# Kernel tuning notes

Measured on AMD Instinct MI355X. Metric: run time of the kernel, lower is better.

Reference implementation:

```python
import jax, jax.numpy as jnp
import numpy as np

OBS_X, OBS_Y, RADIUS = 40.0, 15.0, 6.0
B = 524288  # batch of states


def setup_inputs() -> dict:
    key = jax.random.key(0)
    ks = jax.random.split(key, 14)
    def lin_w(k, o, i):
        return jax.random.normal(k, (o, i), jnp.float32) * (1.0 / np.sqrt(i))
    return {
        "x": jax.random.normal(ks[0], (B, 5), jnp.float32),
        "sgn": 1,
        "mean": jax.random.normal(ks[1], (5,), jnp.float32),
        "std": jax.random.uniform(ks[2], (5,), jnp.float32, minval=0.5, maxval=1.5),
        "fc1_w": lin_w(ks[3], 128, 5),
        "fc1_b": jax.random.normal(ks[4], (128,), jnp.float32) * 0.1,
        "fc21_w": lin_w(ks[5], 32, 128),
        "fc21_b": jax.random.normal(ks[6], (32,), jnp.float32) * 0.1,
        "fc22_w": lin_w(ks[7], 32, 128),
        "fc22_b": jax.random.normal(ks[8], (32,), jnp.float32) * 0.1,
        "fc31_w": lin_w(ks[9], 2, 32),
        "fc31_b": jax.random.normal(ks[10], (2,), jnp.float32) * 0.1,
        "fc32_w": lin_w(ks[11], 2, 32),
        "fc32_b": jax.random.normal(ks[12], (2,), jnp.float32) * 0.1,
    }


def reference(x, sgn, mean, std, fc1_w, fc1_b, fc21_w, fc21_b,
              fc22_w, fc22_b, fc31_w, fc31_b, fc32_w, fc32_b):
    # --- tiny MLP (DynamicUnicycle2D config: 5 -> 128 -> {32,32} -> {2,2}) ---
    x0 = x * std + mean                                   # de-normalized state [B,5]
    h1 = jax.nn.relu(x @ fc1_w.T + fc1_b)                 # [B,128]
    x21 = jax.nn.relu(h1 @ fc21_w.T + fc21_b)             # [B,32]
    x22 = jax.nn.relu(h1 @ fc22_w.T + fc22_b)             # [B,32]
    x31 = x21 @ fc31_w.T + fc31_b                         # QP linear cost p, [B,2]
    x32 = 4.0 * jax.nn.sigmoid(x22 @ fc32_w.T + fc32_b)   # CBF class-K gains, [B,2]

    # --- CBF derivation (relative degree 2, circular obstacle) ---
    px, py, theta, v = x0[:, 0], x0[:, 1], x0[:, 2], x0[:, 3]
    s, c = jnp.sin(theta), jnp.cos(theta)
    dx, dy = px - OBS_X, py - OBS_Y
    barrier = dx * dx + dy * dy - RADIUS * RADIUS
    barrier_dot = 2.0 * dx * v * c + 2.0 * dy * v * s
    Lf2b = 2.0 * v * v
    LgLfbu1 = -2.0 * dx * v * s + 2.0 * dy * v * c
    LgLfbu2 = 2.0 * dx * c + 2.0 * dy * s
    G = jnp.stack([-LgLfbu1, -LgLfbu2], axis=1)           # [B,2], single row constraint
    h = Lf2b + (x32[:, 0] + x32[:, 1]) * barrier_dot + x32[:, 0] * x32[:, 1] * barrier  # [B]

    # --- batched QP: min 0.5 u^T u + p^T u  s.t.  G u <= h  (Q = I, one constraint)
    # Exact KKT solution: project unconstrained optimum onto the half-space.
    u0 = -x31                                             # unconstrained optimum
    viol = jnp.sum(G * u0, axis=1) - h                    # [B]
    gg = jnp.sum(G * G, axis=1)                           # [B]
    lam = jnp.maximum(viol, 0.0) / (gg + 1e-12)           # active-set multiplier
    u = u0 - lam[:, None] * G                             # [B,2] safe control
    return u
```

## Files before the change

### kernel.cpp

```cpp
#include <hip/hip_runtime.h>
#include <hip/hip_bf16.h>
#include <math.h>

typedef __attribute__((ext_vector_type(8))) _Float16 half8;
typedef __attribute__((ext_vector_type(2))) _Float16 half2v;
typedef __attribute__((ext_vector_type(4))) float f32x4;

#define OBS_X 40.0f
#define OBS_Y 15.0f
#define RADIUS 6.0f
#define TPW 16
#define GRID 512

__device__ __forceinline__ half2v pkrtz(float a, float b) {
    return __builtin_bit_cast(half2v, __builtin_amdgcn_cvt_pkrtz(a, b));
}

__device__ __forceinline__ void split8(const float* v, half8& hi, half8& lo) {
#pragma unroll
    for (int j = 0; j < 8; ++j) {
        _Float16 h = (_Float16)v[j];
        hi[j] = h;
        lo[j] = (_Float16)(v[j] - (float)h);
    }
}

__device__ __forceinline__ void pin(half8& v) {
    f32x4 t = __builtin_bit_cast(f32x4, v);
    asm volatile("" : "+v"(t));
    v = __builtin_bit_cast(half8, t);
}

__global__ __launch_bounds__(256, 2) void barriernet_fused(
    const float* __restrict__ x,
    const float* __restrict__ mean_, const float* __restrict__ std_,
    const float* __restrict__ w1,  const float* __restrict__ b1,
    const float* __restrict__ w21, const float* __restrict__ b21,
    const float* __restrict__ w22, const float* __restrict__ b22,
    const float* __restrict__ w31, const float* __restrict__ b31,
    const float* __restrict__ w32, const float* __restrict__ b32,
    float* __restrict__ out)
{
    __shared__ unsigned char smem[36880];
    const int tid  = threadIdx.x;
    const int lane = tid & 63;
    const int wv   = tid >> 6;
    const int r16  = lane & 15;
    const int g    = lane >> 4;
    unsigned char* h1hi = smem + wv * 8192;
    unsigned char* h1lo = h1hi + 4096;
    const unsigned swz = ((unsigned)(r16 & 7)) << 4;
    const int slot = blockIdx.x * 4 + wv;

    if (tid < 128) {
        float v[8];
#pragma unroll
        for (int j = 0; j < 5; ++j) v[j] = w1[tid * 5 + j];
        v[5] = b1[tid];
        v[6] = 0.f; v[7] = 0.f;
        half8 hi, lo;
        split8(v, hi, lo);
        *(half8*)(smem + 32768 + tid * 16) = hi;
        *(half8*)(smem + 34816 + tid * 16) = lo;
    }
    if (tid == 128) {
        half8 z = {0,0,0,0,0,0,0,0};
        *(half8*)(smem + 36864) = z;
    }

    half8 w2h[4][4], w2l[4][4];
#pragma unroll
    for (int t = 0; t < 4; ++t) {
        const int r = 16 * t + r16;
        const float* src = (r < 32) ? (w21 + r * 128) : (w22 + (r - 32) * 128);
#pragma unroll
        for (int kc = 0; kc < 4; ++kc) {
            const float4 f0 = *(const float4*)(src + kc * 32 + g * 8);
            const float4 f1 = *(const float4*)(src + kc * 32 + g * 8 + 4);
            float v[8];
            v[0] = f0.x; v[1] = f0.y; v[2] = f0.z; v[3] = f0.w;
            v[4] = f1.x; v[5] = f1.y; v[6] = f1.z; v[7] = f1.w;
            split8(v, w2h[t][kc], w2l[t][kc]);
            pin(w2h[t][kc]);
            pin(w2l[t][kc]);
        }
    }

    __syncthreads();

    const float m0 = mean_[0], m1 = mean_[1], m2 = mean_[2], m3 = mean_[3];
    const float sd0 = std_[0], sd1 = std_[1], sd2 = std_[2], sd3 = std_[3];
    const float bb31_0 = b31[0], bb31_1 = b31[1], bb32_0 = b32[0], bb32_1 = b32[1];

    const unsigned awbase = (g < 2) ? 32768u : ((g == 2) ? 34816u : 36864u);
    const unsigned awstep = (g == 3) ? 0u : 16u;

    float xa0, xa1, xa2, xa3, xa4;
    {
        const float* xr = x + (size_t)(slot * TPW * 16 + r16) * 5;
        xa0 = xr[0]; xa1 = xr[1]; xa2 = xr[2]; xa3 = xr[3]; xa4 = xr[4];
    }

#pragma unroll 1
    for (int it = 0; it < TPW; ++it) {
        const int rowbase = (slot * TPW + it) * 16;

        half8 bx = {0,0,0,0,0,0,0,0};
        {
            float xs[5] = {xa0, xa1, xa2, xa3, xa4};
            const bool useL = (g == 1), useZ = (g == 3);
#pragma unroll
            for (int j = 0; j < 5; ++j) {
                _Float16 h = (_Float16)xs[j];
                _Float16 l = (_Float16)(xs[j] - (float)h);
                bx[j] = useZ ? (_Float16)0.f : (useL ? l : h);
            }
            bx[5] = (useZ || useL) ? (_Float16)0.f : (_Float16)1.0f;
        }
        const float xc0 = xa0, xc1 = xa1, xc2 = xa2, xc3 = xa3;

        if (it + 1 < TPW) {
            const float* xr = x + (size_t)(rowbase + 16 + r16) * 5;
            xa0 = xr[0]; xa1 = xr[1]; xa2 = xr[2]; xa3 = xr[3]; xa4 = xr[4];
        }

#pragma unroll
        for (int t8 = 0; t8 < 8; ++t8) {
            const int fr = t8 * 16 + r16;
            const half8 aw = *(const half8*)(smem + awbase + (unsigned)fr * awstep);
            f32x4 acc = {0.f, 0.f, 0.f, 0.f};
            acc = __builtin_amdgcn_mfma_f32_16x16x32_f16(aw, bx, acc, 0, 0, 0);
            float v0 = fmaxf(acc[0], 0.f), v1 = fmaxf(acc[1], 0.f);
            float v2 = fmaxf(acc[2], 0.f), v3 = fmaxf(acc[3], 0.f);
            half2v hA = pkrtz(v0, v1);
            half2v hB = pkrtz(v2, v3);
            half2v lA = pkrtz(v0 - (float)hA[0], v1 - (float)hA[1]);
            half2v lB = pkrtz(v2 - (float)hB[0], v3 - (float)hB[1]);
            const unsigned off = ((unsigned)(32 * t8 + 8 * g)) ^ swz;
            uint2 ph; ph.x = __builtin_bit_cast(unsigned, hA); ph.y = __builtin_bit_cast(unsigned, hB);
            uint2 pl; pl.x = __builtin_bit_cast(unsigned, lA); pl.y = __builtin_bit_cast(unsigned, lB);
            *(uint2*)(h1hi + r16 * 256 + off) = ph;
            *(uint2*)(h1lo + r16 * 256 + off) = pl;
        }

        asm volatile("" ::: "memory");

        half8 ah[4], al[4];
#pragma unroll
        for (int kc = 0; kc < 4; ++kc) {
            const unsigned off = ((unsigned)(kc * 64 + g * 16)) ^ swz;
            ah[kc] = *(const half8*)(h1hi + r16 * 256 + off);
            al[kc] = *(const half8*)(h1lo + r16 * 256 + off);
        }
        f32x4 acc2[4];
#pragma unroll
        for (int t = 0; t < 4; ++t) {
            const float4 bb2 = (t < 2) ? *(const float4*)(b21 + 16 * t + 4 * g)
                                       : *(const float4*)(b22 + 16 * (t - 2) + 4 * g);
            f32x4 a = {bb2.x, bb2.y, bb2.z, bb2.w};
#pragma unroll
            for (int kc = 0; kc < 4; ++kc) {
                a = __builtin_amdgcn_mfma_f32_16x16x32_f16(w2h[t][kc], al[kc], a, 0, 0, 0);
                a = __builtin_amdgcn_mfma_f32_16x16x32_f16(w2l[t][kc], ah[kc], a, 0, 0, 0);
                a = __builtin_amdgcn_mfma_f32_16x16x32_f16(w2h[t][kc], ah[kc], a, 0, 0, 0);
            }
            acc2[t] = a;
        }

        asm volatile("" ::: "memory");

        const f32x4 wA0 = *(const f32x4*)(w31 + 4 * g);
        const f32x4 wA1 = *(const f32x4*)(w31 + 16 + 4 * g);
        const f32x4 wB0 = *(const f32x4*)(w31 + 32 + 4 * g);
        const f32x4 wB1 = *(const f32x4*)(w31 + 48 + 4 * g);
        const f32x4 wC0 = *(const f32x4*)(w32 + 4 * g);
        const f32x4 wC1 = *(const f32x4*)(w32 + 16 + 4 * g);
        const f32x4 wD0 = *(const f32x4*)(w32 + 32 + 4 * g);
        const f32x4 wD1 = *(const f32x4*)(w32 + 48 + 4 * g);
        float p0 = 0.f, p1 = 0.f, p2 = 0.f, p3 = 0.f;
#pragma unroll
        for (int r = 0; r < 4; ++r) {
            float v0 = fmaxf(acc2[0][r], 0.f), v1 = fmaxf(acc2[1][r], 0.f);
            float v2 = fmaxf(acc2[2][r], 0.f), v3 = fmaxf(acc2[3][r], 0.f);
            p0 += wA0[r] * v0 + wA1[r] * v1;
            p1 += wB0[r] * v0 + wB1[r] * v1;
            p2 += wC0[r] * v2 + wC1[r] * v3;
            p3 += wD0[r] * v2 + wD1[r] * v3;
        }
        p0 += __shfl_xor(p0, 16); p0 += __shfl_xor(p0, 32);
        p1 += __shfl_xor(p1, 16); p1 += __shfl_xor(p1, 32);
        p2 += __shfl_xor(p2, 16); p2 += __shfl_xor(p2, 32);
        p3 += __shfl_xor(p3, 16); p3 += __shfl_xor(p3, 32);

        if (lane < 16) {
            const float a31_0 = p0 + bb31_0, a31_1 = p1 + bb31_1;
            const float a32_0 = p2 + bb32_0, a32_1 = p3 + bb32_1;
            const float s0 = 4.0f / (1.0f + __expf(-a32_0));
            const float s1 = 4.0f / (1.0f + __expf(-a32_1));
            const float px = fmaf(xc0, sd0, m0);
            const float py = fmaf(xc1, sd1, m1);
            const float th = fmaf(xc2, sd2, m2);
            const float v  = fmaf(xc3, sd3, m3);
            float sn, cs; __sincosf(th, &sn, &cs);
            const float dx = px - OBS_X, dy = py - OBS_Y;
            const float barrier     = dx * dx + dy * dy - RADIUS * RADIUS;
            const float barrier_dot = 2.f * dx * v * cs + 2.f * dy * v * sn;
            const float Lf2b = 2.f * v * v;
            const float G0 = 2.f * dx * v * sn - 2.f * dy * v * cs;
            const float G1 = -(2.f * dx * cs + 2.f * dy * sn);
            const float h  = Lf2b + (s0 + s1) * barrier_dot + s0 * s1 * barrier;
            const float u00 = -a31_0, u01 = -a31_1;
            const float viol = G0 * u00 + G1 * u01 - h;
            const float gg   = G0 * G0 + G1 * G1;
            const float lam  = fmaxf(viol, 0.f) / (gg + 1e-12f);
            float2 uo = make_float2(fmaf(-lam, G0, u00), fmaf(-lam, G1, u01));
            ((float2*)out)[rowbase + r16] = uo;
        }
    }
}

extern "C" void kernel_launch(void* const* d_in, const int* in_sizes, int n_in,
                              void* d_out, int out_size, void* d_ws, size_t ws_size,
                              hipStream_t stream) {
    const float* x     = (const float*)d_in[0];
    const float* mean_ = (const float*)d_in[2];
    const float* std_  = (const float*)d_in[3];
    const float* w1    = (const float*)d_in[4];
    const float* b1    = (const float*)d_in[5];
    const float* w21   = (const float*)d_in[6];
    const float* b21   = (const float*)d_in[7];
    const float* w22   = (const float*)d_in[8];
    const float* b22   = (const float*)d_in[9];
    const float* w31   = (const float*)d_in[10];
    const float* b31   = (const float*)d_in[11];
    const float* w32   = (const float*)d_in[12];
    const float* b32   = (const float*)d_in[13];

    barriernet_fused<<<GRID, 256, 0, stream>>>(
        x, mean_, std_, w1, b1, w21, b21, w22, b22, w31, b31, w32, b32,
        (float*)d_out);
}
```

Baseline: 133.6 us.

## Move fc2 low-half weights to LDS, raise occupancy, batch epilogue across four tiles

```diff
diff --git a/kernel.cpp b/kernel.cpp
--- a/kernel.cpp
+++ b/kernel.cpp
@@ -9,8 +9,8 @@
 #define OBS_X 40.0f
 #define OBS_Y 15.0f
 #define RADIUS 6.0f
-#define TPW 16
-#define GRID 512
+#define TPW 8
+#define GRID 1024
 
 __device__ __forceinline__ half2v pkrtz(float a, float b) {
     return __builtin_bit_cast(half2v, __builtin_amdgcn_cvt_pkrtz(a, b));
@@ -31,7 +31,7 @@
     v = __builtin_bit_cast(half8, t);
 }
 
-__global__ __launch_bounds__(256, 2) void barriernet_fused(
+__global__ __launch_bounds__(256, 3) void barriernet_fused(
     const float* __restrict__ x,
     const float* __restrict__ mean_, const float* __restrict__ std_,
     const float* __restrict__ w1,  const float* __restrict__ b1,
@@ -41,7 +41,7 @@
     const float* __restrict__ w32, const float* __restrict__ b32,
     float* __restrict__ out)
 {
-    __shared__ unsigned char smem[36880];
+    __shared__ unsigned char smem[53264];
     const int tid  = threadIdx.x;
     const int lane = tid & 63;
     const int wv   = tid >> 6;
@@ -60,15 +60,30 @@
         v[6] = 0.f; v[7] = 0.f;
         half8 hi, lo;
         split8(v, hi, lo);
-        *(half8*)(smem + 32768 + tid * 16) = hi;
-        *(half8*)(smem + 34816 + tid * 16) = lo;
+        *(half8*)(smem + 49152 + tid * 16) = hi;
+        *(half8*)(smem + 51200 + tid * 16) = lo;
     }
     if (tid == 128) {
         half8 z = {0,0,0,0,0,0,0,0};
-        *(half8*)(smem + 36864) = z;
-    }
-
-    half8 w2h[4][4], w2l[4][4];
+        *(half8*)(smem + 53248) = z;
+    }
+
+#pragma unroll
+    for (int m = 0; m < 4; ++m) {
+        const int s = tid * 4 + m;
+        const int f = s >> 6, l = s & 63;
+        const int r = 16 * (f >> 2) + (l & 15);
+        const int k0 = (f & 3) * 32 + (l >> 4) * 8;
+        const float* src = (r < 32) ? (w21 + r * 128 + k0) : (w22 + (r - 32) * 128 + k0);
+        const float4 f0 = *(const float4*)(src);
+        const float4 f1 = *(const float4*)(src + 4);
+        float v[8] = {f0.x, f0.y, f0.z, f0.w, f1.x, f1.y, f1.z, f1.w};
+        half8 hi, lo;
+        split8(v, hi, lo);
+        *(half8*)(smem + 32768 + s * 16) = lo;
+    }
+
+    half8 w2h[4][4];
 #pragma unroll
     for (int t = 0; t < 4; ++t) {
         const int r = 16 * t + r16;
@@ -77,12 +92,10 @@
         for (int kc = 0; kc < 4; ++kc) {
             const float4 f0 = *(const float4*)(src + kc * 32 + g * 8);
             const float4 f1 = *(const float4*)(src + kc * 32 + g * 8 + 4);
-            float v[8];
-            v[0] = f0.x; v[1] = f0.y; v[2] = f0.z; v[3] = f0.w;
-            v[4] = f1.x; v[5] = f1.y; v[6] = f1.z; v[7] = f1.w;
-            split8(v, w2h[t][kc], w2l[t][kc]);
+            float v[8] = {f0.x, f0.y, f0.z, f0.w, f1.x, f1.y, f1.z, f1.w};
+#pragma unroll
+            for (int j = 0; j < 8; ++j) w2h[t][kc][j] = (_Float16)v[j];
             pin(w2h[t][kc]);
-            pin(w2l[t][kc]);
         }
     }
 
@@ -92,14 +105,17 @@
     const float sd0 = std_[0], sd1 = std_[1], sd2 = std_[2], sd3 = std_[3];
     const float bb31_0 = b31[0], bb31_1 = b31[1], bb32_0 = b32[0], bb32_1 = b32[1];
 
-    const unsigned awbase = (g < 2) ? 32768u : ((g == 2) ? 34816u : 36864u);
+    const unsigned awbase = (g < 2) ? 49152u : ((g == 2) ? 51200u : 53248u);
     const unsigned awstep = (g == 3) ? 0u : 16u;
+    const unsigned w2lbase = 32768u + (unsigned)lane * 16u;
 
     float xa0, xa1, xa2, xa3, xa4;
     {
         const float* xr = x + (size_t)(slot * TPW * 16 + r16) * 5;
         xa0 = xr[0]; xa1 = xr[1]; xa2 = xr[2]; xa3 = xr[3]; xa4 = xr[4];
     }
+
+    float P0 = 0.f, P1 = 0.f, P2 = 0.f, P3 = 0.f;
 
 #pragma unroll 1
     for (int it = 0; it < TPW; ++it) {
@@ -117,7 +133,6 @@
             }
             bx[5] = (useZ || useL) ? (_Float16)0.f : (_Float16)1.0f;
         }
-        const float xc0 = xa0, xc1 = xa1, xc2 = xa2, xc3 = xa3;
 
         if (it + 1 < TPW) {
             const float* xr = x + (size_t)(rowbase + 16 + r16) * 5;
@@ -160,8 +175,9 @@
             f32x4 a = {bb2.x, bb2.y, bb2.z, bb2.w};
 #pragma unroll
             for (int kc = 0; kc < 4; ++kc) {
+                const half8 wl = *(const half8*)(smem + w2lbase + (unsigned)((t * 4 + kc) << 10));
                 a = __builtin_amdgcn_mfma_f32_16x16x32_f16(w2h[t][kc], al[kc], a, 0, 0, 0);
-                a = __builtin_amdgcn_mfma_f32_16x16x32_f16(w2l[t][kc], ah[kc], a, 0, 0, 0);
+                a = __builtin_amdgcn_mfma_f32_16x16x32_f16(wl,         ah[kc], a, 0, 0, 0);
                 a = __builtin_amdgcn_mfma_f32_16x16x32_f16(w2h[t][kc], ah[kc], a, 0, 0, 0);
             }
             acc2[t] = a;
@@ -192,15 +208,26 @@
         p2 += __shfl_xor(p2, 16); p2 += __shfl_xor(p2, 32);
         p3 += __shfl_xor(p3, 16); p3 += __shfl_xor(p3, 32);
 
-        if (lane < 16) {
-            const float a31_0 = p0 + bb31_0, a31_1 = p1 + bb31_1;
-            const float a32_0 = p2 + bb32_0, a32_1 = p3 + bb32_1;
+        {
+            const bool sel = (g == (it & 3));
+            P0 = sel ? p0 : P0;
+            P1 = sel ? p1 : P1;
+            P2 = sel ? p2 : P2;
+            P3 = sel ? p3 : P3;
+        }
+
+        if ((it & 3) == 3) {
+            const int row = (slot * TPW + (it - 3)) * 16 + lane;
+            const float* xr = x + (size_t)row * 5;
+            const float e0 = xr[0], e1 = xr[1], e2 = xr[2], e3 = xr[3];
+            const float a31_0 = P0 + bb31_0, a31_1 = P1 + bb31_1;
+            const float a32_0 = P2 + bb32_0, a32_1 = P3 + bb32_1;
             const float s0 = 4.0f / (1.0f + __expf(-a32_0));
             const float s1 = 4.0f / (1.0f + __expf(-a32_1));
-            const float px = fmaf(xc0, sd0, m0);
-            const float py = fmaf(xc1, sd1, m1);
-            const float th = fmaf(xc2, sd2, m2);
-            const float v  = fmaf(xc3, sd3, m3);
+            const float px = fmaf(e0, sd0, m0);
+            const float py = fmaf(e1, sd1, m1);
+            const float th = fmaf(e2, sd2, m2);
+            const float v  = fmaf(e3, sd3, m3);
             float sn, cs; __sincosf(th, &sn, &cs);
             const float dx = px - OBS_X, dy = py - OBS_Y;
             const float barrier     = dx * dx + dy * dy - RADIUS * RADIUS;
@@ -214,7 +241,7 @@
             const float gg   = G0 * G0 + G1 * G1;
             const float lam  = fmaxf(viol, 0.f) / (gg + 1e-12f);
             float2 uo = make_float2(fmaf(-lam, G0, u00), fmaf(-lam, G1, u01));
-            ((float2*)out)[rowbase + r16] = uo;
+            ((float2*)out)[row] = uo;
         }
     }
 }
```

After: 146.0 us. +9.2%, slower.

## Double-buffer fc1 activations in LDS to overlap next tile's fc1 with fc2

Applied to the files above, without the earlier changes.

```diff
diff --git a/kernel.cpp b/kernel.cpp
--- a/kernel.cpp
+++ b/kernel.cpp
@@ -41,14 +41,13 @@
     const float* __restrict__ w32, const float* __restrict__ b32,
     float* __restrict__ out)
 {
-    __shared__ unsigned char smem[36880];
+    __shared__ unsigned char smem[69648];
     const int tid  = threadIdx.x;
     const int lane = tid & 63;
     const int wv   = tid >> 6;
     const int r16  = lane & 15;
     const int g    = lane >> 4;
-    unsigned char* h1hi = smem + wv * 8192;
-    unsigned char* h1lo = h1hi + 4096;
+    unsigned char* h1base = smem + wv * 16384;
     const unsigned swz = ((unsigned)(r16 & 7)) << 4;
     const int slot = blockIdx.x * 4 + wv;
 
@@ -60,12 +59,12 @@
         v[6] = 0.f; v[7] = 0.f;
         half8 hi, lo;
         split8(v, hi, lo);
-        *(half8*)(smem + 32768 + tid * 16) = hi;
-        *(half8*)(smem + 34816 + tid * 16) = lo;
+        *(half8*)(smem + 65536 + tid * 16) = hi;
+        *(half8*)(smem + 67584 + tid * 16) = lo;
     }
     if (tid == 128) {
         half8 z = {0,0,0,0,0,0,0,0};
-        *(half8*)(smem + 36864) = z;
+        *(half8*)(smem + 69632) = z;
     }
 
     half8 w2h[4][4], w2l[4][4];
@@ -92,56 +91,71 @@
     const float sd0 = std_[0], sd1 = std_[1], sd2 = std_[2], sd3 = std_[3];
     const float bb31_0 = b31[0], bb31_1 = b31[1], bb32_0 = b32[0], bb32_1 = b32[1];
 
-    const unsigned awbase = (g < 2) ? 32768u : ((g == 2) ? 34816u : 36864u);
+    const unsigned awbase = (g < 2) ? 65536u : ((g == 2) ? 67584u : 69632u);
     const unsigned awstep = (g == 3) ? 0u : 16u;
+
+#define FC1_TO(BUF, BX)                                                               \
+    {                                                                                 \
+        unsigned char* hhi = h1base + ((unsigned)(BUF) << 13);                        \
+        unsigned char* hlo = hhi + 4096;                                              \
+        _Pragma("unroll")                                                             \
+        for (int t8 = 0; t8 < 8; ++t8) {                                              \
+            const int fr = t8 * 16 + r16;                                             \
+            const half8 aw = *(const half8*)(smem + awbase + (unsigned)fr * awstep);  \
+            f32x4 acc = {0.f, 0.f, 0.f, 0.f};                                         \
+            acc = __builtin_amdgcn_mfma_f32_16x16x32_f16(aw, BX, acc, 0, 0, 0);       \
+            float v0 = fmaxf(acc[0], 0.f), v1 = fmaxf(acc[1], 0.f);                   \
+            float v2 = fmaxf(acc[2], 0.f), v3 = fmaxf(acc[3], 0.f);                   \
+            half2v hA = pkrtz(v0, v1);                                                \
+            half2v hB = pkrtz(v2, v3);                                                \
+            half2v lA = pkrtz(v0 - (float)hA[0], v1 - (float)hA[1]);                  \
+            half2v lB = pkrtz(v2 - (float)hB[0], v3 - (float)hB[1]);                  \
+            const unsigned off = ((unsigned)(32 * t8 + 8 * g)) ^ swz;                 \
+            uint2 ph; ph.x = __builtin_bit_cast(unsigned, hA);                        \
+            ph.y = __builtin_bit_cast(unsigned, hB);                                  \
+            uint2 pl; pl.x = __builtin_bit_cast(unsigned, lA);                        \
+            pl.y = __builtin_bit_cast(unsigned, lB);                                  \
+            *(uint2*)(hhi + r16 * 256 + off) = ph;                                    \
+            *(uint2*)(hlo + r16 * 256 + off) = pl;                                    \
+        }                                                                             \
+    }
+
+#define BUILD_BX(DST, X0, X1, X2, X3, X4)                                             \
+    {                                                                                 \
+        float xs[5] = {X0, X1, X2, X3, X4};                                           \
+        const bool useL = (g == 1), useZ = (g == 3);                                  \
+        _Pragma("unroll")                                                             \
+        for (int j = 0; j < 5; ++j) {                                                 \
+            _Float16 h = (_Float16)xs[j];                                             \
+            _Float16 l = (_Float16)(xs[j] - (float)h);                                \
+            DST[j] = useZ ? (_Float16)0.f : (useL ? l : h);                           \
+        }                                                                             \
+        DST[5] = (useZ || useL) ? (_Float16)0.f : (_Float16)1.0f;                     \
+        DST[6] = (_Float16)0.f; DST[7] = (_Float16)0.f;                               \
+    }
 
     float xa0, xa1, xa2, xa3, xa4;
     {
         const float* xr = x + (size_t)(slot * TPW * 16 + r16) * 5;
         xa0 = xr[0]; xa1 = xr[1]; xa2 = xr[2]; xa3 = xr[3]; xa4 = xr[4];
     }
+    float xc0 = xa0, xc1 = xa1, xc2 = xa2, xc3 = xa3;
+    {
+        half8 bx0;
+        BUILD_BX(bx0, xa0, xa1, xa2, xa3, xa4);
+        FC1_TO(0, bx0);
+    }
+    {
+        const float* xr = x + (size_t)(slot * TPW * 16 + 16 + r16) * 5;
+        xa0 = xr[0]; xa1 = xr[1]; xa2 = xr[2]; xa3 = xr[3]; xa4 = xr[4];
+    }
 
 #pragma unroll 1
     for (int it = 0; it < TPW; ++it) {
+        const int cur = it & 1;
         const int rowbase = (slot * TPW + it) * 16;
-
-        half8 bx = {0,0,0,0,0,0,0,0};
-        {
-            float xs[5] = {xa0, xa1, xa2, xa3, xa4};
-            const bool useL = (g == 1), useZ = (g == 3);
-#pragma unroll
-            for (int j = 0; j < 5; ++j) {
-                _Float16 h = (_Float16)xs[j];
-                _Float16 l = (_Float16)(xs[j] - (float)h);
-                bx[j] = useZ ? (_Float16)0.f : (useL ? l : h);
-            }
-            bx[5] = (useZ || useL) ? (_Float16)0.f : (_Float16)1.0f;
-        }
-        const float xc0 = xa0, xc1 = xa1, xc2 = xa2, xc3 = xa3;
-
-        if (it + 1 < TPW) {
-            const float* xr = x + (size_t)(rowbase + 16 + r16) * 5;
-            xa0 = xr[0]; xa1 = xr[1]; xa2 = xr[2]; xa3 = xr[3]; xa4 = xr[4];
-        }
-
-#pragma unroll
-        for (int t8 = 0; t8 < 8; ++t8) {
-            const int fr = t8 * 16 + r16;
-            const half8 aw = *(const half8*)(smem + awbase + (unsigned)fr * awstep);
-            f32x4 acc = {0.f, 0.f, 0.f, 0.f};
-            acc = __builtin_amdgcn_mfma_f32_16x16x32_f16(aw, bx, acc, 0, 0, 0);
-            float v0 = fmaxf(acc[0], 0.f), v1 = fmaxf(acc[1], 0.f);
-            float v2 = fmaxf(acc[2], 0.f), v3 = fmaxf(acc[3], 0.f);
-            half2v hA = pkrtz(v0, v1);
-            half2v hB = pkrtz(v2, v3);
-            half2v lA = pkrtz(v0 - (float)hA[0], v1 - (float)hA[1]);
-            half2v lB = pkrtz(v2 - (float)hB[0], v3 - (float)hB[1]);
-            const unsigned off = ((unsigned)(32 * t8 + 8 * g)) ^ swz;
-            uint2 ph; ph.x = __builtin_bit_cast(unsigned, hA); ph.y = __builtin_bit_cast(unsigned, hB);
-            uint2 pl; pl.x = __builtin_bit_cast(unsigned, lA); pl.y = __builtin_bit_cast(unsigned, lB);
-            *(uint2*)(h1hi + r16 * 256 + off) = ph;
-            *(uint2*)(h1lo + r16 * 256 + off) = pl;
-        }
+        unsigned char* bhi = h1base + ((unsigned)cur << 13);
+        unsigned char* blo = bhi + 4096;
 
         asm volatile("" ::: "memory");
 
@@ -149,9 +163,22 @@
 #pragma unroll
         for (int kc = 0; kc < 4; ++kc) {
             const unsigned off = ((unsigned)(kc * 64 + g * 16)) ^ swz;
-            ah[kc] = *(const half8*)(h1hi + r16 * 256 + off);
-            al[kc] = *(const half8*)(h1lo + r16 * 256 + off);
-        }
+            ah[kc] = *(const half8*)(bhi + r16 * 256 + off);
+            al[kc] = *(const half8*)(blo + r16 * 256 + off);
+        }
+
+        float xn0 = xc0, xn1 = xc1, xn2 = xc2, xn3 = xc3;
+        if (it + 1 < TPW) {
+            xn0 = xa0; xn1 = xa1; xn2 = xa2; xn3 = xa3;
+            half8 bxn;
+            BUILD_BX(bxn, xa0, xa1, xa2, xa3, xa4);
+            if (it + 2 < TPW) {
+                const float* xr = x + (size_t)(rowbase + 32 + r16) * 5;
+                xa0 = xr[0]; xa1 = xr[1]; xa2 = xr[2]; xa3 = xr[3]; xa4 = xr[4];
+            }
+            FC1_TO(cur ^ 1, bxn);
+        }
+
         f32x4 acc2[4];
 #pragma unroll
         for (int t = 0; t < 4; ++t) {
@@ -166,8 +193,6 @@
             }
             acc2[t] = a;
         }
-
-        asm volatile("" ::: "memory");
 
         const f32x4 wA0 = *(const f32x4*)(w31 + 4 * g);
         const f32x4 wA1 = *(const f32x4*)(w31 + 16 + 4 * g);
@@ -216,7 +241,11 @@
             float2 uo = make_float2(fmaf(-lam, G0, u00), fmaf(-lam, G1, u01));
             ((float2*)out)[rowbase + r16] = uo;
         }
-    }
+
+        xc0 = xn0; xc1 = xn1; xc2 = xn2; xc3 = xn3;
+    }
+#undef FC1_TO
+#undef BUILD_BX
 }
 
 extern "C" void kernel_launch(void* const* d_in, const int* in_sizes, int n_in,
```

New measurement: 137.4 us. 2.8% more time.
